# Optimization experiments

Measured on AMD Instinct MI355X. Metric: run time of the kernel, lower is better.

## Reference

```python
import jax, jax.numpy as jnp
import numpy as np

DIM = 768
NUM_HEADS = 12
HEAD_DIM = DIM // NUM_HEADS
SCALE = HEAD_DIM ** -0.5


def setup_inputs() -> dict:
    key = jax.random.key(0)
    ks = jax.random.split(key, 9)
    B, N = 2, 4096
    s = DIM ** -0.5
    return {
        "query": jax.random.normal(ks[0], (B, N, DIM), jnp.float32),
        "key": jax.random.normal(ks[1], (B, N, DIM), jnp.float32),
        "value": jax.random.normal(ks[2], (B, N, DIM), jnp.float32),
        "Wq": jax.random.normal(ks[3], (DIM, DIM), jnp.float32) * s,
        "Wk": jax.random.normal(ks[4], (DIM, DIM), jnp.float32) * s,
        "bk": jax.random.normal(ks[5], (DIM,), jnp.float32) * 0.02,
        "Wv": jax.random.normal(ks[6], (DIM, DIM), jnp.float32) * s,
        "Wp": jax.random.normal(ks[7], (DIM, DIM), jnp.float32) * s,
        "bp": jax.random.normal(ks[8], (DIM,), jnp.float32) * 0.02,
    }


def reference(query, key, value, Wq, Wk, bk, Wv, Wp, bp):
    B, Nq, C = query.shape
    Nk = key.shape[1]
    H, D = NUM_HEADS, HEAD_DIM
    # QKV projections (qv_bias=False -> no bias on q, v; k has bias)
    q = (query @ Wq.T).reshape(B, Nq, H, D).transpose(0, 2, 1, 3)  # [B,H,Nq,D]
    k = (key @ Wk.T + bk).reshape(B, Nk, H, D).transpose(0, 2, 1, 3)
    v = (value @ Wv.T).reshape(B, Nk, H, D).transpose(0, 2, 1, 3)
    # non-standard: exact GELU applied to K before QK^T
    k = jax.nn.gelu(k, approximate=False)
    attn = jnp.einsum("bhqd,bhkd->bhqk", q, k) * SCALE
    attn = jax.nn.softmax(attn, axis=-1)
    x = jnp.einsum("bhqk,bhkd->bhqd", attn, v)
    x = x.transpose(0, 2, 1, 3).reshape(B, Nq, C)
    return x @ Wp.T + bp
```

## Files before the change

### kernel.cpp

```cpp
#include <hip/hip_runtime.h>
#include <hip/hip_bf16.h>


#define DIM 768
#define NH 12
#define HD 64
#define NTOK 4096
#define WELEM 589824u
#define TELEM 6291456u

typedef short bf16x8 __attribute__((ext_vector_type(8)));
typedef float floatx4 __attribute__((ext_vector_type(4)));
typedef unsigned short us4 __attribute__((ext_vector_type(4)));

__device__ __forceinline__ float bf2f(unsigned short u) {
    union { unsigned int i; float f; } v; v.i = ((unsigned int)u) << 16; return v.f;
}
__device__ __forceinline__ unsigned short f2bf(float f) {
    union { float f; unsigned int i; } v; v.f = f;
    unsigned int r = v.i + 0x7fffu + ((v.i >> 16) & 1u);
    return (unsigned short)(r >> 16);
}
__device__ __forceinline__ unsigned int packbf(float a, float b) {
    __hip_bfloat162 h = __float22bfloat162_rn(make_float2(a, b));
    union { __hip_bfloat162 h; unsigned int u; } cv; cv.h = h; return cv.u;
}
__device__ __forceinline__ void gl2lds16(const unsigned short* g, unsigned short* l) {
    __builtin_amdgcn_global_load_lds(
        (const __attribute__((address_space(1))) unsigned int*)g,
        (__attribute__((address_space(3))) unsigned int*)l, 16, 0, 0);
}
__device__ __forceinline__ bf16x8 ld8_f32_to_bf16(const float* p) {
    floatx4 f0 = *(const floatx4*)p;
    floatx4 f1 = *(const floatx4*)(p + 4);
    union { unsigned int u[4]; bf16x8 v; } o;
    o.u[0] = packbf(f0[0], f0[1]);
    o.u[1] = packbf(f0[2], f0[3]);
    o.u[2] = packbf(f1[0], f1[1]);
    o.u[3] = packbf(f1[2], f1[3]);
    return o.v;
}

#if __has_builtin(__builtin_amdgcn_exp2f)
#define EXPFN(x) __builtin_amdgcn_exp2f(x)
#define QSCALE 0.18033688011f
#else
#define EXPFN(x) __expf(x)
#define QSCALE 0.125f
#endif

__global__ __launch_bounds__(256) void cvt_w(
    const float* __restrict__ a, const float* __restrict__ b,
    const float* __restrict__ c, const float* __restrict__ d,
    unsigned short* __restrict__ dst)
{
    size_t i = ((size_t)blockIdx.x * 256 + threadIdx.x) * 8;
    const float* s; size_t off;
    if (i < WELEM)            { s = a; off = i; }
    else if (i < 2u * WELEM)  { s = b; off = i - WELEM; }
    else if (i < 3u * WELEM)  { s = c; off = i - 2u * WELEM; }
    else                      { s = d; off = i - 3u * WELEM; }
    *(bf16x8*)(dst + i) = ld8_f32_to_bf16(s + off);
}

__global__ __launch_bounds__(256) void cvt_in(
    const float* __restrict__ a, const float* __restrict__ b,
    const float* __restrict__ c, unsigned short* __restrict__ dst)
{
    size_t i = ((size_t)blockIdx.x * 256 + threadIdx.x) * 8;
    const float* s; size_t off;
    if (i < TELEM)            { s = a; off = i; }
    else if (i < 2u * TELEM)  { s = b; off = i - TELEM; }
    else                      { s = c; off = i - 2u * TELEM; }
    *(bf16x8*)(dst + i) = ld8_f32_to_bf16(s + off);
}

template <int A_IS_BF16>
__device__ __forceinline__ void gemm128(
    const void* __restrict__ Av, const unsigned short* __restrict__ W,
    const float* __restrict__ bias, void* __restrict__ Cv,
    int has_bias, int do_gelu, int trans, int out_f32)
{
    __shared__ unsigned short As[128 * 64];
    __shared__ unsigned short Bs[128 * 64];
    const int m0 = blockIdx.x * 128, n0 = blockIdx.y * 128;
    const int tid = threadIdx.x;
    const int w = tid >> 6, l = tid & 63;
    const int g = l >> 4, r16 = l & 15;
    const int wm = w >> 1, wn = w & 1;
    const int ro = l >> 3, c = l & 7;
    const int cswz = ((c ^ ro) & 7) * 8;

    floatx4 acc[4][4];
#pragma unroll
    for (int i = 0; i < 4; i++)
#pragma unroll
        for (int j = 0; j < 4; j++) acc[i][j] = (floatx4){0.f, 0.f, 0.f, 0.f};

    for (int k0 = 0; k0 < DIM; k0 += 64) {
#pragma unroll
        for (int q = 0; q < 4; q++) {
            int rbase = w * 32 + q * 8;
            if (A_IS_BF16) {
                gl2lds16((const unsigned short*)Av + (size_t)(m0 + rbase + ro) * DIM + k0 + cswz,
                         As + rbase * 64);
            } else {
                bf16x8 a = ld8_f32_to_bf16((const float*)Av + (size_t)(m0 + rbase + ro) * DIM + k0 + c * 8);
                *(bf16x8*)(As + (rbase + ro) * 64 + cswz) = a;
            }
            gl2lds16(W + (size_t)(n0 + rbase + ro) * DIM + k0 + cswz, Bs + rbase * 64);
        }
        __syncthreads();

#pragma unroll
        for (int kk = 0; kk < 2; kk++) {
            bf16x8 af[4], bfr[4];
            int x = r16 & 7;
#pragma unroll
            for (int i = 0; i < 4; i++)
                af[i] = *(const bf16x8*)(As + (wm * 64 + i * 16 + r16) * 64 + (((kk * 4 + g) ^ x) * 8));
#pragma unroll
            for (int j = 0; j < 4; j++)
                bfr[j] = *(const bf16x8*)(Bs + (wn * 64 + j * 16 + r16) * 64 + (((kk * 4 + g) ^ x) * 8));
#pragma unroll
            for (int i = 0; i < 4; i++)
#pragma unroll
                for (int j = 0; j < 4; j++)
                    acc[i][j] = __builtin_amdgcn_mfma_f32_16x16x32_bf16(af[i], bfr[j], acc[i][j], 0, 0, 0);
        }
        __syncthreads();
    }

    if (trans) {
        unsigned short* C = (unsigned short*)Cv;
#pragma unroll
        for (int i = 0; i < 4; i++) {
            int m = m0 + wm * 64 + i * 16 + g * 4;
            int b = m >> 12, tloc = m & 4095;
#pragma unroll
            for (int j = 0; j < 4; j++) {
                int n = n0 + wn * 64 + j * 16 + r16;
                int h = n >> 6, d = n & 63;
                union { unsigned int u[2]; us4 v; } pk;
                pk.u[0] = packbf(acc[i][j][0], acc[i][j][1]);
                pk.u[1] = packbf(acc[i][j][2], acc[i][j][3]);
                *(us4*)(C + ((size_t)(b * NH + h) * 64 + d) * NTOK + tloc) = pk.v;
            }
        }
    } else {
#pragma unroll
        for (int i = 0; i < 4; i++)
#pragma unroll
            for (int j = 0; j < 4; j++) {
                int n = n0 + wn * 64 + j * 16 + r16;
                float bv = has_bias ? bias[n] : 0.f;
#pragma unroll
                for (int r = 0; r < 4; r++) {
                    int m = m0 + wm * 64 + i * 16 + g * 4 + r;
                    float v = acc[i][j][r] + bv;
                    if (do_gelu) v = 0.5f * v * (1.f + erff(v * 0.70710678118f));
                    if (out_f32) ((float*)Cv)[(size_t)m * DIM + n] = v;
                    else ((unsigned short*)Cv)[(size_t)m * DIM + n] = f2bf(v);
                }
            }
    }
}

template <int A_IS_BF16>
__global__ __launch_bounds__(256) void qkv_gemm(
    const void* __restrict__ q_in, const void* __restrict__ k_in,
    const void* __restrict__ v_in,
    const unsigned short* __restrict__ Wq, const unsigned short* __restrict__ Wk,
    const unsigned short* __restrict__ Wv, const float* __restrict__ bk,
    unsigned short* __restrict__ Qo, unsigned short* __restrict__ Ko,
    unsigned short* __restrict__ Vto)
{
    int z = blockIdx.z;
    const void* A = (z == 0) ? q_in : (z == 1) ? k_in : v_in;
    const unsigned short* W = (z == 0) ? Wq : (z == 1) ? Wk : Wv;
    unsigned short* C = (z == 0) ? Qo : (z == 1) ? Ko : Vto;
    gemm128<A_IS_BF16>(A, W, bk, C, z == 1, z == 1, z == 2, 0);
}

__global__ __launch_bounds__(256) void out_gemm(
    const unsigned short* __restrict__ X, const unsigned short* __restrict__ Wp,
    const float* __restrict__ bp, float* __restrict__ out)
{
    gemm128<1>(X, Wp, bp, out, 1, 0, 0, 1);
}

__device__ __forceinline__ int swzf(int R) { return (R & 7) ^ ((R >> 2) & 6); }

__global__ __launch_bounds__(256, 3) void attn_kernel(
    const unsigned short* __restrict__ Q, const unsigned short* __restrict__ K,
    const unsigned short* __restrict__ Vt, unsigned short* __restrict__ X)
{
    __shared__ unsigned short Ks[2][64 * 64];
    __shared__ unsigned short Vs[2][64 * 64];
    const int qt = blockIdx.x, bh = blockIdx.y;
    const int b = bh / NH, h = bh % NH;
    const int tid = threadIdx.x;
    const int w = tid >> 6, l = tid & 63;
    const int g = l >> 4, r16 = l & 15;
    const int tokbase = b * NTOK;

    bf16x8 qfr[2][2];
#pragma unroll
    for (int qfi = 0; qfi < 2; qfi++) {
        int qrow = tokbase + qt * 128 + w * 32 + qfi * 16 + r16;
#pragma unroll
        for (int kk = 0; kk < 2; kk++) {
            bf16x8 t = *(const bf16x8*)(Q + (size_t)qrow * DIM + h * HD + kk * 32 + g * 8);
#pragma unroll
            for (int j = 0; j < 8; j++)
                t[j] = (short)f2bf(bf2f((unsigned short)t[j]) * QSCALE);
            qfr[qfi][kk] = t;
        }
    }

    int koff[4][2], voff[4][2];
#pragma unroll
    for (int ct = 0; ct < 4; ct++) {
        int krow = (ct >> 1) * 32 + (r16 >> 2) * 8 + (ct & 1) * 4 + (r16 & 3);
#pragma unroll
        for (int kk = 0; kk < 2; kk++)
            koff[ct][kk] = krow * 64 + (((kk * 4 + g) ^ swzf(krow)) * 8);
    }
#pragma unroll
    for (int dt = 0; dt < 4; dt++) {
        int vrow = dt * 16 + r16;
#pragma unroll
        for (int c = 0; c < 2; c++)
            voff[dt][c] = vrow * 64 + (((c * 4 + g) ^ swzf(vrow)) * 8);
    }

    const int kv = w >> 1, half = w & 1;
    int soff[4];
    const int srl = l >> 3, scc = l & 7;
    const int sstride = (kv == 0) ? DIM : NTOK;
#pragma unroll
    for (int i = 0; i < 4; i++) {
        int row = half * 32 + i * 8 + srl;
        soff[i] = row * sstride + ((scc ^ swzf(row)) * 8);
    }
    const unsigned short* Kbase = K + (size_t)tokbase * DIM + h * HD;
    const unsigned short* Vbase = Vt + (size_t)bh * 64 * NTOK;

    floatx4 o[2][4];
#pragma unroll
    for (int qfi = 0; qfi < 2; qfi++)
#pragma unroll
        for (int dt = 0; dt < 4; dt++) o[qfi][dt] = (floatx4){0.f, 0.f, 0.f, 0.f};
    float lsum[2] = {0.f, 0.f};

    {
        const unsigned short* p = (kv == 0) ? Kbase : Vbase;
        unsigned short* dst = ((kv == 0) ? Ks[0] : Vs[0]) + half * 2048;
#pragma unroll
        for (int i = 0; i < 4; i++) gl2lds16(p + soff[i], dst + i * 512);
    }

    for (int kt = 0; kt < NTOK / 64; kt++) {
        const int cur = kt & 1;
        __syncthreads();

        bf16x8 kr[4][2], vr[4][2];
#pragma unroll
        for (int ct = 0; ct < 4; ct++)
#pragma unroll
            for (int kk = 0; kk < 2; kk++)
                kr[ct][kk] = *(const bf16x8*)(Ks[cur] + koff[ct][kk]);
#pragma unroll
        for (int dt = 0; dt < 4; dt++)
#pragma unroll
            for (int c = 0; c < 2; c++)
                vr[dt][c] = *(const bf16x8*)(Vs[cur] + voff[dt][c]);

        if (kt + 1 < NTOK / 64) {
            int keyg = (kt + 1) * 64;
            const unsigned short* p = (kv == 0) ? (Kbase + (size_t)keyg * DIM)
                                                : (Vbase + keyg);
            unsigned short* dst = ((kv == 0) ? Ks[cur ^ 1] : Vs[cur ^ 1]) + half * 2048;
#pragma unroll
            for (int i = 0; i < 4; i++) gl2lds16(p + soff[i], dst + i * 512);
        }

#pragma unroll
        for (int qfi = 0; qfi < 2; qfi++) {
            floatx4 s[4];
#pragma unroll
            for (int ct = 0; ct < 4; ct++) {
                floatx4 zz = (floatx4){0.f, 0.f, 0.f, 0.f};
                zz = __builtin_amdgcn_mfma_f32_16x16x32_bf16(kr[ct][0], qfr[qfi][0], zz, 0, 0, 0);
                s[ct] = __builtin_amdgcn_mfma_f32_16x16x32_bf16(kr[ct][1], qfr[qfi][1], zz, 0, 0, 0);
            }
            float ls0 = 0.f, ls1 = 0.f, ls2 = 0.f, ls3 = 0.f;
#pragma unroll
            for (int ct = 0; ct < 4; ct++) {
                float p0 = EXPFN(s[ct][0]);
                float p1 = EXPFN(s[ct][1]);
                float p2 = EXPFN(s[ct][2]);
                float p3 = EXPFN(s[ct][3]);
                s[ct][0] = p0; s[ct][1] = p1; s[ct][2] = p2; s[ct][3] = p3;
                ls0 += p0; ls1 += p1; ls2 += p2; ls3 += p3;
            }
            lsum[qfi] += (ls0 + ls1) + (ls2 + ls3);

            unsigned int pk[4][2];
#pragma unroll
            for (int ct = 0; ct < 4; ct++) {
                pk[ct][0] = packbf(s[ct][0], s[ct][1]);
                pk[ct][1] = packbf(s[ct][2], s[ct][3]);
            }
#pragma unroll
            for (int c = 0; c < 2; c++) {
                union { unsigned int u[4]; bf16x8 v; } bf;
                bf.u[0] = pk[2 * c][0]; bf.u[1] = pk[2 * c][1];
                bf.u[2] = pk[2 * c + 1][0]; bf.u[3] = pk[2 * c + 1][1];
#pragma unroll
                for (int dt = 0; dt < 4; dt++)
                    o[qfi][dt] = __builtin_amdgcn_mfma_f32_16x16x32_bf16(vr[dt][c], bf.v, o[qfi][dt], 0, 0, 0);
            }
        }
    }

#pragma unroll
    for (int qfi = 0; qfi < 2; qfi++) {
        lsum[qfi] += __shfl_xor(lsum[qfi], 16, 64);
        lsum[qfi] += __shfl_xor(lsum[qfi], 32, 64);
    }

#pragma unroll
    for (int qfi = 0; qfi < 2; qfi++) {
        float inv = 1.f / lsum[qfi];
        int tok = tokbase + qt * 128 + w * 32 + qfi * 16 + r16;
#pragma unroll
        for (int dt = 0; dt < 4; dt++) {
            union { unsigned int u[2]; us4 v; } pkv;
            pkv.u[0] = packbf(o[qfi][dt][0] * inv, o[qfi][dt][1] * inv);
            pkv.u[1] = packbf(o[qfi][dt][2] * inv, o[qfi][dt][3] * inv);
            *(us4*)(X + (size_t)tok * DIM + h * HD + dt * 16 + g * 4) = pkv.v;
        }
    }
}

extern "C" void kernel_launch(void* const* d_in, const int* in_sizes, int n_in,
                              void* d_out, int out_size, void* d_ws, size_t ws_size,
                              hipStream_t stream) {
    const float* query = (const float*)d_in[0];
    const float* key   = (const float*)d_in[1];
    const float* value = (const float*)d_in[2];
    const float* Wq    = (const float*)d_in[3];
    const float* Wk    = (const float*)d_in[4];
    const float* bk    = (const float*)d_in[5];
    const float* Wv    = (const float*)d_in[6];
    const float* Wp    = (const float*)d_in[7];
    const float* bp    = (const float*)d_in[8];
    float* out = (float*)d_out;

    unsigned short* ws = (unsigned short*)d_ws;
    unsigned short* Wqb = ws;
    unsigned short* Wkb = Wqb + WELEM;
    unsigned short* Wvb = Wkb + WELEM;
    unsigned short* Wpb = Wvb + WELEM;
    unsigned short* Qp  = Wpb + WELEM;
    unsigned short* Kp  = Qp + TELEM;
    unsigned short* Vtp = Kp + TELEM;
    unsigned short* Xp  = Vtp + TELEM;
    unsigned short* Qbf = Xp + TELEM;
    unsigned short* Kbf = Qbf + TELEM;
    unsigned short* Vbf = Kbf + TELEM;

    const size_t base_b = ((size_t)4 * WELEM + 4 * TELEM) * 2;
    const size_t cvt_b  = (size_t)3 * TELEM * 2;
    const bool cvt_ok = ws_size >= base_b + cvt_b;

    cvt_w<<<dim3(4 * WELEM / 8 / 256), 256, 0, stream>>>(Wq, Wk, Wv, Wp, Wqb);
    if (cvt_ok) {
        cvt_in<<<dim3(3 * TELEM / 8 / 256), 256, 0, stream>>>(query, key, value, Qbf);
        qkv_gemm<1><<<dim3(64, 6, 3), 256, 0, stream>>>(Qbf, Kbf, Vbf, Wqb, Wkb, Wvb, bk, Qp, Kp, Vtp);
    } else {
        qkv_gemm<0><<<dim3(64, 6, 3), 256, 0, stream>>>(query, key, value, Wqb, Wkb, Wvb, bk, Qp, Kp, Vtp);
    }
    attn_kernel<<<dim3(32, 24), 256, 0, stream>>>(Qp, Kp, Vtp, Xp);
    out_gemm<<<dim3(64, 6), 256, 0, stream>>>(Xp, Wpb, bp, out);
}
```

Measured before the change: 311.2 us.

## Split attention work across 8 waves with 16 query rows each

Restructures the attention kernel so each wave processes 16 query rows instead of 32, doubling the block to 512 threads while keeping the 128-row query tile. K/V tile staging is split four ways per tensor instead of two. This lowers per-wave register use to raise occupancy and latency hiding. The trade-off is that each K/V LDS fragment is read by twice as many waves, raising LDS read traffic relative to MFMA work.

```diff
diff --git a/kernel.cpp b/kernel.cpp
--- a/kernel.cpp
+++ b/kernel.cpp
@@ -191,7 +191,7 @@
 
 __device__ __forceinline__ int swzf(int R) { return (R & 7) ^ ((R >> 2) & 6); }
 
-__global__ __launch_bounds__(256, 3) void attn_kernel(
+__global__ __launch_bounds__(512, 6) void attn_kernel(
     const unsigned short* __restrict__ Q, const unsigned short* __restrict__ K,
     const unsigned short* __restrict__ Vt, unsigned short* __restrict__ X)
 {
@@ -204,17 +204,16 @@
     const int g = l >> 4, r16 = l & 15;
     const int tokbase = b * NTOK;
 
-    bf16x8 qfr[2][2];
-#pragma unroll
-    for (int qfi = 0; qfi < 2; qfi++) {
-        int qrow = tokbase + qt * 128 + w * 32 + qfi * 16 + r16;
+    bf16x8 qfr[2];
+    {
+        int qrow = tokbase + qt * 128 + w * 16 + r16;
 #pragma unroll
         for (int kk = 0; kk < 2; kk++) {
             bf16x8 t = *(const bf16x8*)(Q + (size_t)qrow * DIM + h * HD + kk * 32 + g * 8);
 #pragma unroll
             for (int j = 0; j < 8; j++)
                 t[j] = (short)f2bf(bf2f((unsigned short)t[j]) * QSCALE);
-            qfr[qfi][kk] = t;
+            qfr[kk] = t;
         }
     }
 
@@ -234,30 +233,28 @@
             voff[dt][c] = vrow * 64 + (((c * 4 + g) ^ swzf(vrow)) * 8);
     }
 
-    const int kv = w >> 1, half = w & 1;
-    int soff[4];
+    const int kv = w >> 2, quarter = w & 3;
+    int soff[2];
     const int srl = l >> 3, scc = l & 7;
     const int sstride = (kv == 0) ? DIM : NTOK;
 #pragma unroll
-    for (int i = 0; i < 4; i++) {
-        int row = half * 32 + i * 8 + srl;
+    for (int i = 0; i < 2; i++) {
+        int row = quarter * 16 + i * 8 + srl;
         soff[i] = row * sstride + ((scc ^ swzf(row)) * 8);
     }
     const unsigned short* Kbase = K + (size_t)tokbase * DIM + h * HD;
     const unsigned short* Vbase = Vt + (size_t)bh * 64 * NTOK;
 
-    floatx4 o[2][4];
-#pragma unroll
-    for (int qfi = 0; qfi < 2; qfi++)
-#pragma unroll
-        for (int dt = 0; dt < 4; dt++) o[qfi][dt] = (floatx4){0.f, 0.f, 0.f, 0.f};
-    float lsum[2] = {0.f, 0.f};
+    floatx4 o[4];
+#pragma unroll
+    for (int dt = 0; dt < 4; dt++) o[dt] = (floatx4){0.f, 0.f, 0.f, 0.f};
+    float lsum = 0.f;
 
     {
         const unsigned short* p = (kv == 0) ? Kbase : Vbase;
-        unsigned short* dst = ((kv == 0) ? Ks[0] : Vs[0]) + half * 2048;
-#pragma unroll
-        for (int i = 0; i < 4; i++) gl2lds16(p + soff[i], dst + i * 512);
+        unsigned short* dst = ((kv == 0) ? Ks[0] : Vs[0]) + quarter * 1024;
+#pragma unroll
+        for (int i = 0; i < 2; i++) gl2lds16(p + soff[i], dst + i * 512);
     }
 
     for (int kt = 0; kt < NTOK / 64; kt++) {
@@ -280,65 +277,58 @@
             int keyg = (kt + 1) * 64;
             const unsigned short* p = (kv == 0) ? (Kbase + (size_t)keyg * DIM)
                                                 : (Vbase + keyg);
-            unsigned short* dst = ((kv == 0) ? Ks[cur ^ 1] : Vs[cur ^ 1]) + half * 2048;
-#pragma unroll
-            for (int i = 0; i < 4; i++) gl2lds16(p + soff[i], dst + i * 512);
-        }
-
-#pragma unroll
-        for (int qfi = 0; qfi < 2; qfi++) {
-            floatx4 s[4];
-#pragma unroll
-            for (int ct = 0; ct < 4; ct++) {
-                floatx4 zz = (floatx4){0.f, 0.f, 0.f, 0.f};
-                zz = __builtin_amdgcn_mfma_f32_16x16x32_bf16(kr[ct][0], qfr[qfi][0], zz, 0, 0, 0);
-                s[ct] = __builtin_amdgcn_mfma_f32_16x16x32_bf16(kr[ct][1], qfr[qfi][1], zz, 0, 0, 0);
-            }
-            float ls0 = 0.f, ls1 = 0.f, ls2 = 0.f, ls3 = 0.f;
-#pragma unroll
-            for (int ct = 0; ct < 4; ct++) {
-                float p0 = EXPFN(s[ct][0]);
-                float p1 = EXPFN(s[ct][1]);
-                float p2 = EXPFN(s[ct][2]);
-                float p3 = EXPFN(s[ct][3]);
-                s[ct][0] = p0; s[ct][1] = p1; s[ct][2] = p2; s[ct][3] = p3;
-                ls0 += p0; ls1 += p1; ls2 += p2; ls3 += p3;
-            }
-            lsum[qfi] += (ls0 + ls1) + (ls2 + ls3);
-
-            unsigned int pk[4][2];
-#pragma unroll
-            for (int ct = 0; ct < 4; ct++) {
-                pk[ct][0] = packbf(s[ct][0], s[ct][1]);
-                pk[ct][1] = packbf(s[ct][2], s[ct][3]);
-            }
-#pragma unroll
-            for (int c = 0; c < 2; c++) {
-                union { unsigned int u[4]; bf16x8 v; } bf;
-                bf.u[0] = pk[2 * c][0]; bf.u[1] = pk[2 * c][1];
-                bf.u[2] = pk[2 * c + 1][0]; bf.u[3] = pk[2 * c + 1][1];
-#pragma unroll
-                for (int dt = 0; dt < 4; dt++)
-                    o[qfi][dt] = __builtin_amdgcn_mfma_f32_16x16x32_bf16(vr[dt][c], bf.v, o[qfi][dt], 0, 0, 0);
-            }
-        }
-    }
-
-#pragma unroll
-    for (int qfi = 0; qfi < 2; qfi++) {
-        lsum[qfi] += __shfl_xor(lsum[qfi], 16, 64);
-        lsum[qfi] += __shfl_xor(lsum[qfi], 32, 64);
-    }
-
-#pragma unroll
-    for (int qfi = 0; qfi < 2; qfi++) {
-        float inv = 1.f / lsum[qfi];
-        int tok = tokbase + qt * 128 + w * 32 + qfi * 16 + r16;
+            unsigned short* dst = ((kv == 0) ? Ks[cur ^ 1] : Vs[cur ^ 1]) + quarter * 1024;
+#pragma unroll
+            for (int i = 0; i < 2; i++) gl2lds16(p + soff[i], dst + i * 512);
+        }
+
+        floatx4 s[4];
+#pragma unroll
+        for (int ct = 0; ct < 4; ct++) {
+            floatx4 zz = (floatx4){0.f, 0.f, 0.f, 0.f};
+            zz = __builtin_amdgcn_mfma_f32_16x16x32_bf16(kr[ct][0], qfr[0], zz, 0, 0, 0);
+            s[ct] = __builtin_amdgcn_mfma_f32_16x16x32_bf16(kr[ct][1], qfr[1], zz, 0, 0, 0);
+        }
+        float ls0 = 0.f, ls1 = 0.f, ls2 = 0.f, ls3 = 0.f;
+#pragma unroll
+        for (int ct = 0; ct < 4; ct++) {
+            float p0 = EXPFN(s[ct][0]);
+            float p1 = EXPFN(s[ct][1]);
+            float p2 = EXPFN(s[ct][2]);
+            float p3 = EXPFN(s[ct][3]);
+            s[ct][0] = p0; s[ct][1] = p1; s[ct][2] = p2; s[ct][3] = p3;
+            ls0 += p0; ls1 += p1; ls2 += p2; ls3 += p3;
+        }
+        lsum += (ls0 + ls1) + (ls2 + ls3);
+
+        unsigned int pk[4][2];
+#pragma unroll
+        for (int ct = 0; ct < 4; ct++) {
+            pk[ct][0] = packbf(s[ct][0], s[ct][1]);
+            pk[ct][1] = packbf(s[ct][2], s[ct][3]);
+        }
+#pragma unroll
+        for (int c = 0; c < 2; c++) {
+            union { unsigned int u[4]; bf16x8 v; } bf;
+            bf.u[0] = pk[2 * c][0]; bf.u[1] = pk[2 * c][1];
+            bf.u[2] = pk[2 * c + 1][0]; bf.u[3] = pk[2 * c + 1][1];
+#pragma unroll
+            for (int dt = 0; dt < 4; dt++)
+                o[dt] = __builtin_amdgcn_mfma_f32_16x16x32_bf16(vr[dt][c], bf.v, o[dt], 0, 0, 0);
+        }
+    }
+
+    lsum += __shfl_xor(lsum, 16, 64);
+    lsum += __shfl_xor(lsum, 32, 64);
+
+    {
+        float inv = 1.f / lsum;
+        int tok = tokbase + qt * 128 + w * 16 + r16;
 #pragma unroll
         for (int dt = 0; dt < 4; dt++) {
             union { unsigned int u[2]; us4 v; } pkv;
-            pkv.u[0] = packbf(o[qfi][dt][0] * inv, o[qfi][dt][1] * inv);
-            pkv.u[1] = packbf(o[qfi][dt][2] * inv, o[qfi][dt][3] * inv);
+            pkv.u[0] = packbf(o[dt][0] * inv, o[dt][1] * inv);
+            pkv.u[1] = packbf(o[dt][2] * inv, o[dt][3] * inv);
             *(us4*)(X + (size_t)tok * DIM + h * HD + dt * 16 + g * 4) = pkv.v;
         }
     }
@@ -382,6 +372,6 @@
     } else {
         qkv_gemm<0><<<dim3(64, 6, 3), 256, 0, stream>>>(query, key, value, Wqb, Wkb, Wvb, bk, Qp, Kp, Vtp);
     }
-    attn_kernel<<<dim3(32, 24), 256, 0, stream>>>(Qp, Kp, Vtp, Xp);
+    attn_kernel<<<dim3(32, 24), 512, 0, stream>>>(Qp, Kp, Vtp, Xp);
     out_gemm<<<dim3(64, 6), 256, 0, stream>>>(Xp, Wpb, bp, out);
 }
```

Result: slower. 951.3 us (+205.6%).
